# Kernel tuning notes

Hardware: AMD Instinct MI355X
Metric: run time of the kernel (lower is better)

Reference implementation:

```python
import jax, jax.numpy as jnp
import numpy as np

B, N, C, C_OUT, E = 8, 1024, 256, 256, 16384


def setup_inputs() -> dict:
    key = jax.random.key(0)
    k1, k2, k3 = jax.random.split(key, 3)
    x = jax.random.normal(k1, (B, N, C), dtype=jnp.float32)
    edge_index = jax.random.randint(k2, (2, E, B), 0, N)  # [2, E, B], values in [0, N)
    W = jax.random.normal(k3, (C_OUT, C), dtype=jnp.float32) * 0.02  # torch Linear weight [out, in]
    b = jnp.zeros((C_OUT,), dtype=jnp.float32)
    return {"x": x, "edge_index": edge_index, "W": W, "b": b}


def reference(x, edge_index, W, b):
    Bs, Nn, Cc = x.shape
    BN = Bs * Nn
    # Vectorized version of the per-batch python loop: offset each graph's
    # node indices into the big block-diagonal adjacency.
    offs = jnp.arange(Bs, dtype=edge_index.dtype) * Nn          # [B]
    src = (edge_index[0] + offs[None, :]).reshape(-1)           # [E*B]
    dst = (edge_index[1] + offs[None, :]).reshape(-1)           # [E*B]
    adj = jnp.zeros((BN, BN), dtype=x.dtype).at[src, dst].set(1.0)
    adj = adj + jnp.eye(BN, dtype=x.dtype)                      # self loops (adds on top, as in torch code)
    D = adj.sum(axis=1)                                         # [BN]
    d_inv_sqrt = jnp.where(D > 0, jax.lax.rsqrt(D), 0.0)        # pow(-0.5) with inf -> 0
    adj_n = d_inv_sqrt[:, None] * adj * d_inv_sqrt[None, :]     # D^-1/2 A D^-1/2
    h = adj_n @ x.reshape(BN, Cc)                               # [BN, C]
    out = h @ W.T + b                                           # Linear
    return out.reshape(Bs, Nn, -1)
```

## Files before the change

### kernel.cpp

```cpp
#include <hip/hip_runtime.h>
#include <stdint.h>

#define B_   8
#define N_   1024
#define C_   256
#define E_   16384
#define BN_  (B_ * N_)
#define NW_  (N_ / 32)
#define LIST_CAP 96

typedef __attribute__((ext_vector_type(8))) short bf16x8;
typedef __attribute__((ext_vector_type(4))) float f32x4;

static __device__ __forceinline__ short f32_to_bf16(float f) {
  uint32_t u = __float_as_uint(f);
  uint32_t r = (u + 0x7fffu + ((u >> 16) & 1u)) >> 16;
  return (short)r;
}
static __device__ __forceinline__ float bf16_to_f32(short s) {
  return __uint_as_float(((uint32_t)(uint16_t)s) << 16);
}

__global__ __launch_bounds__(256) void gemm_scatter(
    const float* __restrict__ X, const float* __restrict__ W,
    const int* __restrict__ ei, uint32_t* __restrict__ mask,
    float* __restrict__ Y) {
  __shared__ __attribute__((aligned(16))) short Ah[64][40];
  __shared__ __attribute__((aligned(16))) short Al[64][40];
  __shared__ __attribute__((aligned(16))) short Bh[64][40];
  __shared__ __attribute__((aligned(16))) short Bl[64][40];

  int t  = threadIdx.x;
  int m0 = blockIdx.x * 64;
  int n0 = blockIdx.y * 64;

  {
    int e   = (blockIdx.y * gridDim.x + blockIdx.x) * 256 + t;
    int b   = e & (B_ - 1);
    int src = ei[e];
    int dst = ei[E_ * B_ + e];
    atomicOr(&mask[(size_t)(b * N_ + src) * NW_ + (dst >> 5)],
             1u << (dst & 31));
  }

  int lr = t >> 2;
  int lc = (t & 3) * 8;
  int wv = t >> 6;
  int ln = t & 63;
  int lm = ln & 15;
  int qd = ln >> 4;

  f32x4 acc[4];
#pragma unroll
  for (int i = 0; i < 4; i++) acc[i] = (f32x4){0.f, 0.f, 0.f, 0.f};

  for (int k0 = 0; k0 < C_; k0 += 32) {
    const float* xr = &X[(size_t)(m0 + lr) * C_ + k0 + lc];
    const float* wr = &W[(size_t)(n0 + lr) * C_ + k0 + lc];
    float xv[8], wv8[8];
    *(float4*)&xv[0] = *(const float4*)&xr[0];
    *(float4*)&xv[4] = *(const float4*)&xr[4];
    *(float4*)&wv8[0] = *(const float4*)&wr[0];
    *(float4*)&wv8[4] = *(const float4*)&wr[4];
    bf16x8 xh, xl, wh, wl;
#pragma unroll
    for (int j = 0; j < 8; j++) {
      short h = f32_to_bf16(xv[j]);
      xh[j] = h;
      xl[j] = f32_to_bf16(xv[j] - bf16_to_f32(h));
      short g = f32_to_bf16(wv8[j]);
      wh[j] = g;
      wl[j] = f32_to_bf16(wv8[j] - bf16_to_f32(g));
    }
    __syncthreads();
    *(bf16x8*)&Ah[lr][lc] = xh;
    *(bf16x8*)&Al[lr][lc] = xl;
    *(bf16x8*)&Bh[lr][lc] = wh;
    *(bf16x8*)&Bl[lr][lc] = wl;
    __syncthreads();

    bf16x8 ah = *(const bf16x8*)&Ah[16 * wv + lm][qd * 8];
    bf16x8 al = *(const bf16x8*)&Al[16 * wv + lm][qd * 8];
#pragma unroll
    for (int nt = 0; nt < 4; nt++) {
      bf16x8 bh = *(const bf16x8*)&Bh[nt * 16 + lm][qd * 8];
      bf16x8 bl = *(const bf16x8*)&Bl[nt * 16 + lm][qd * 8];
      acc[nt] = __builtin_amdgcn_mfma_f32_16x16x32_bf16(ah, bh, acc[nt], 0, 0, 0);
      acc[nt] = __builtin_amdgcn_mfma_f32_16x16x32_bf16(ah, bl, acc[nt], 0, 0, 0);
      acc[nt] = __builtin_amdgcn_mfma_f32_16x16x32_bf16(al, bh, acc[nt], 0, 0, 0);
    }
  }

#pragma unroll
  for (int nt = 0; nt < 4; nt++) {
#pragma unroll
    for (int r = 0; r < 4; r++) {
      int m = m0 + 16 * wv + qd * 4 + r;
      int n = n0 + nt * 16 + lm;
      Y[(size_t)m * C_ + n] = acc[nt][r];
    }
  }
}

__global__ __launch_bounds__(256) void aggregate(
    const uint32_t* __restrict__ mask, const float* __restrict__ Y,
    const float* __restrict__ bias, float* __restrict__ out) {
  __shared__ uint16_t lists[4][LIST_CAP];
  __shared__ float    wgts[4][LIST_CAP];

  int blk   = blockIdx.x;
  int batch = blk & 7;
  int group = blk >> 3;
  int wv    = threadIdx.x >> 6;
  int ln    = threadIdx.x & 63;
  int loc   = group * 4 + wv;
  int node  = batch * N_ + loc;
  int c4    = ln * 4;

  const uint32_t* mb = mask + (size_t)batch * N_ * NW_;

  uint32_t bits = (ln < NW_) ? mb[(size_t)loc * NW_ + ln] : 0u;
  int cnt = __popc(bits);
  int pfx = cnt;
#pragma unroll
  for (int off = 1; off < 64; off <<= 1) {
    int v = __shfl_up(pfx, off);
    if (ln >= off) pfx += v;
  }
  int total = __shfl(pfx, 63);
  pfx -= cnt;
  uint16_t* lst = lists[wv];
  float*    wgt = wgts[wv];
  int o = pfx, jb = ln * 32;
  while (bits) {
    int j = __ffs(bits) - 1;
    bits &= bits - 1;
    lst[o++] = (uint16_t)(jb + j);
  }
  if (ln == 0) {
    int dd = total;
    while (dd & 3) { lst[dd] = 0; wgt[dd] = 0.f; dd++; }
  }

  int half = ln >> 5;
  int wl   = ln & 31;
  for (int k = 0; k < total; k += 2) {
    int kk = k + half;
    int nj = (kk < total) ? lst[kk] : 0;
    int p  = __popc(mb[(size_t)nj * NW_ + wl]);
    p += __shfl_xor(p, 1);  p += __shfl_xor(p, 2);  p += __shfl_xor(p, 4);
    p += __shfl_xor(p, 8);  p += __shfl_xor(p, 16);
    if (wl == 0 && kk < total) wgt[kk] = rsqrtf((float)(p + 1));
  }

  const float* yb = Y + (size_t)batch * N_ * C_;
  float di = rsqrtf((float)(total + 1));
  float4 s = *(const float4*)&yb[(size_t)loc * C_ + c4];
  float4 acc;
  acc.x = di * s.x; acc.y = di * s.y; acc.z = di * s.z; acc.w = di * s.w;

  for (int k = 0; k < total; k += 4) {
    ushort4 n4 = *(const ushort4*)&lst[k];
    float4  w4 = *(const float4*)&wgt[k];
    float4 z0 = *(const float4*)&yb[(size_t)n4.x * C_ + c4];
    float4 z1 = *(const float4*)&yb[(size_t)n4.y * C_ + c4];
    float4 z2 = *(const float4*)&yb[(size_t)n4.z * C_ + c4];
    float4 z3 = *(const float4*)&yb[(size_t)n4.w * C_ + c4];
    acc.x += w4.x * z0.x; acc.y += w4.x * z0.y; acc.z += w4.x * z0.z; acc.w += w4.x * z0.w;
    acc.x += w4.y * z1.x; acc.y += w4.y * z1.y; acc.z += w4.y * z1.z; acc.w += w4.y * z1.w;
    acc.x += w4.z * z2.x; acc.y += w4.z * z2.y; acc.z += w4.z * z2.z; acc.w += w4.z * z2.w;
    acc.x += w4.w * z3.x; acc.y += w4.w * z3.y; acc.z += w4.w * z3.z; acc.w += w4.w * z3.w;
  }

  float4 bb = *(const float4*)&bias[c4];
  float4 o4;
  o4.x = di * acc.x + bb.x;
  o4.y = di * acc.y + bb.y;
  o4.z = di * acc.z + bb.z;
  o4.w = di * acc.w + bb.w;
  *(float4*)&out[(size_t)node * C_ + c4] = o4;
}

extern "C" void kernel_launch(void* const* d_in, const int* in_sizes, int n_in,
                              void* d_out, int out_size, void* d_ws,
                              size_t ws_size, hipStream_t stream) {
  const float* x    = (const float*)d_in[0];
  const int*   ei   = (const int*)d_in[1];
  const float* W    = (const float*)d_in[2];
  const float* bias = (const float*)d_in[3];
  float*       out  = (float*)d_out;

  char* ws = (char*)d_ws;
  uint32_t* mask = (uint32_t*)(ws + 0x000000);
  float*    Y    = (float*)   (ws + 0x100000);

  hipMemsetAsync(mask, 0, (size_t)BN_ * NW_ * 4, stream);

  gemm_scatter<<<dim3(BN_ / 64, C_ / 64), 256, 0, stream>>>(x, W, ei, mask, Y);
  aggregate<<<BN_ / 4, 256, 0, stream>>>(mask, Y, bias, out);
}
```

Measured before the change: 97.29 us.

## Fuse memset, GEMM/scatter and aggregation into one cooperative kernel with grid syncs

Replaces the memset plus two kernel launches with a single cooperative kernel of 512 blocks. Each block first zeroes part of the adjacency bitmask, then does the edge scatter and a GEMM tile, and after a grid sync loops over four virtual aggregation blocks. This removes launch and inter-kernel gaps. In exchange it adds grid-wide barrier costs and cuts the aggregation phase to a fixed 512-block grid with serialized iterations.

```diff
diff --git a/kernel.cpp b/kernel.cpp
--- a/kernel.cpp
+++ b/kernel.cpp
@@ -1,5 +1,8 @@
 #include <hip/hip_runtime.h>
+#include <hip/hip_cooperative_groups.h>
 #include <stdint.h>
+
+namespace cg = cooperative_groups;
 
 #define B_   8
 #define N_   1024
@@ -8,6 +11,7 @@
 #define BN_  (B_ * N_)
 #define NW_  (N_ / 32)
 #define LIST_CAP 96
+#define GRID_ 512
 
 typedef __attribute__((ext_vector_type(8))) short bf16x8;
 typedef __attribute__((ext_vector_type(4))) float f32x4;
@@ -21,28 +25,36 @@
   return __uint_as_float(((uint32_t)(uint16_t)s) << 16);
 }
 
-__global__ __launch_bounds__(256) void gemm_scatter(
+__global__ __launch_bounds__(256, 2) void gcn_fused(
     const float* __restrict__ X, const float* __restrict__ W,
-    const int* __restrict__ ei, uint32_t* __restrict__ mask,
-    float* __restrict__ Y) {
+    const int* __restrict__ ei, const float* __restrict__ bias,
+    uint32_t* __restrict__ mask, float* __restrict__ Y,
+    float* __restrict__ out) {
   __shared__ __attribute__((aligned(16))) short Ah[64][40];
   __shared__ __attribute__((aligned(16))) short Al[64][40];
   __shared__ __attribute__((aligned(16))) short Bh[64][40];
   __shared__ __attribute__((aligned(16))) short Bl[64][40];
-
-  int t  = threadIdx.x;
-  int m0 = blockIdx.x * 64;
-  int n0 = blockIdx.y * 64;
+  __shared__ uint16_t lists[4][LIST_CAP];
+  __shared__ float    wgts[4][LIST_CAP];
+
+  cg::grid_group grid = cg::this_grid();
+  int t   = threadIdx.x;
+  int tid = blockIdx.x * 256 + t;
+
+  ((uint2*)mask)[tid] = make_uint2(0u, 0u);
+  __threadfence();
+  grid.sync();
 
   {
-    int e   = (blockIdx.y * gridDim.x + blockIdx.x) * 256 + t;
-    int b   = e & (B_ - 1);
-    int src = ei[e];
-    int dst = ei[E_ * B_ + e];
+    int b   = tid & (B_ - 1);
+    int src = ei[tid];
+    int dst = ei[E_ * B_ + tid];
     atomicOr(&mask[(size_t)(b * N_ + src) * NW_ + (dst >> 5)],
              1u << (dst & 31));
   }
 
+  int m0 = (blockIdx.x >> 2) * 64;
+  int n0 = (blockIdx.x & 3) * 64;
   int lr = t >> 2;
   int lc = (t & 3) * 8;
   int wv = t >> 6;
@@ -100,85 +112,82 @@
       Y[(size_t)m * C_ + n] = acc[nt][r];
     }
   }
-}
-
-__global__ __launch_bounds__(256) void aggregate(
-    const uint32_t* __restrict__ mask, const float* __restrict__ Y,
-    const float* __restrict__ bias, float* __restrict__ out) {
-  __shared__ uint16_t lists[4][LIST_CAP];
-  __shared__ float    wgts[4][LIST_CAP];
-
-  int blk   = blockIdx.x;
-  int batch = blk & 7;
-  int group = blk >> 3;
-  int wv    = threadIdx.x >> 6;
-  int ln    = threadIdx.x & 63;
-  int loc   = group * 4 + wv;
-  int node  = batch * N_ + loc;
-  int c4    = ln * 4;
-
-  const uint32_t* mb = mask + (size_t)batch * N_ * NW_;
-
-  uint32_t bits = (ln < NW_) ? mb[(size_t)loc * NW_ + ln] : 0u;
-  int cnt = __popc(bits);
-  int pfx = cnt;
-#pragma unroll
-  for (int off = 1; off < 64; off <<= 1) {
-    int v = __shfl_up(pfx, off);
-    if (ln >= off) pfx += v;
-  }
-  int total = __shfl(pfx, 63);
-  pfx -= cnt;
-  uint16_t* lst = lists[wv];
-  float*    wgt = wgts[wv];
-  int o = pfx, jb = ln * 32;
-  while (bits) {
-    int j = __ffs(bits) - 1;
-    bits &= bits - 1;
-    lst[o++] = (uint16_t)(jb + j);
-  }
-  if (ln == 0) {
-    int dd = total;
-    while (dd & 3) { lst[dd] = 0; wgt[dd] = 0.f; dd++; }
-  }
-
-  int half = ln >> 5;
-  int wl   = ln & 31;
-  for (int k = 0; k < total; k += 2) {
-    int kk = k + half;
-    int nj = (kk < total) ? lst[kk] : 0;
-    int p  = __popc(mb[(size_t)nj * NW_ + wl]);
-    p += __shfl_xor(p, 1);  p += __shfl_xor(p, 2);  p += __shfl_xor(p, 4);
-    p += __shfl_xor(p, 8);  p += __shfl_xor(p, 16);
-    if (wl == 0 && kk < total) wgt[kk] = rsqrtf((float)(p + 1));
-  }
-
-  const float* yb = Y + (size_t)batch * N_ * C_;
-  float di = rsqrtf((float)(total + 1));
-  float4 s = *(const float4*)&yb[(size_t)loc * C_ + c4];
-  float4 acc;
-  acc.x = di * s.x; acc.y = di * s.y; acc.z = di * s.z; acc.w = di * s.w;
-
-  for (int k = 0; k < total; k += 4) {
-    ushort4 n4 = *(const ushort4*)&lst[k];
-    float4  w4 = *(const float4*)&wgt[k];
-    float4 z0 = *(const float4*)&yb[(size_t)n4.x * C_ + c4];
-    float4 z1 = *(const float4*)&yb[(size_t)n4.y * C_ + c4];
-    float4 z2 = *(const float4*)&yb[(size_t)n4.z * C_ + c4];
-    float4 z3 = *(const float4*)&yb[(size_t)n4.w * C_ + c4];
-    acc.x += w4.x * z0.x; acc.y += w4.x * z0.y; acc.z += w4.x * z0.z; acc.w += w4.x * z0.w;
-    acc.x += w4.y * z1.x; acc.y += w4.y * z1.y; acc.z += w4.y * z1.z; acc.w += w4.y * z1.w;
-    acc.x += w4.z * z2.x; acc.y += w4.z * z2.y; acc.z += w4.z * z2.z; acc.w += w4.z * z2.w;
-    acc.x += w4.w * z3.x; acc.y += w4.w * z3.y; acc.z += w4.w * z3.z; acc.w += w4.w * z3.w;
-  }
-
-  float4 bb = *(const float4*)&bias[c4];
-  float4 o4;
-  o4.x = di * acc.x + bb.x;
-  o4.y = di * acc.y + bb.y;
-  o4.z = di * acc.z + bb.z;
-  o4.w = di * acc.w + bb.w;
-  *(float4*)&out[(size_t)node * C_ + c4] = o4;
+
+  __threadfence();
+  grid.sync();
+  __threadfence();
+
+  for (int it = 0; it < 4; it++) {
+    int vblk  = it * GRID_ + blockIdx.x;
+    int batch = vblk & 7;
+    int group = vblk >> 3;
+    int loc   = group * 4 + wv;
+    int node  = batch * N_ + loc;
+    int c4    = ln * 4;
+
+    const uint32_t* mb = mask + (size_t)batch * N_ * NW_;
+
+    uint32_t bits = (ln < NW_) ? mb[(size_t)loc * NW_ + ln] : 0u;
+    int cnt = __popc(bits);
+    int pfx = cnt;
+#pragma unroll
+    for (int off = 1; off < 64; off <<= 1) {
+      int v = __shfl_up(pfx, off);
+      if (ln >= off) pfx += v;
+    }
+    int total = __shfl(pfx, 63);
+    pfx -= cnt;
+    uint16_t* lst = lists[wv];
+    float*    wgt = wgts[wv];
+    int o = pfx, jb = ln * 32;
+    while (bits) {
+      int j = __ffs(bits) - 1;
+      bits &= bits - 1;
+      lst[o++] = (uint16_t)(jb + j);
+    }
+    if (ln == 0) {
+      int dd = total;
+      while (dd & 3) { lst[dd] = 0; wgt[dd] = 0.f; dd++; }
+    }
+
+    int half = ln >> 5;
+    int wl   = ln & 31;
+    for (int k = 0; k < total; k += 2) {
+      int kk = k + half;
+      int nj = (kk < total) ? lst[kk] : 0;
+      int p  = __popc(mb[(size_t)nj * NW_ + wl]);
+      p += __shfl_xor(p, 1);  p += __shfl_xor(p, 2);  p += __shfl_xor(p, 4);
+      p += __shfl_xor(p, 8);  p += __shfl_xor(p, 16);
+      if (wl == 0 && kk < total) wgt[kk] = rsqrtf((float)(p + 1));
+    }
+
+    const float* yb = Y + (size_t)batch * N_ * C_;
+    float di = rsqrtf((float)(total + 1));
+    float4 s = *(const float4*)&yb[(size_t)loc * C_ + c4];
+    float4 a4;
+    a4.x = di * s.x; a4.y = di * s.y; a4.z = di * s.z; a4.w = di * s.w;
+
+    for (int k = 0; k < total; k += 4) {
+      ushort4 n4 = *(const ushort4*)&lst[k];
+      float4  w4 = *(const float4*)&wgt[k];
+      float4 z0 = *(const float4*)&yb[(size_t)n4.x * C_ + c4];
+      float4 z1 = *(const float4*)&yb[(size_t)n4.y * C_ + c4];
+      float4 z2 = *(const float4*)&yb[(size_t)n4.z * C_ + c4];
+      float4 z3 = *(const float4*)&yb[(size_t)n4.w * C_ + c4];
+      a4.x += w4.x * z0.x; a4.y += w4.x * z0.y; a4.z += w4.x * z0.z; a4.w += w4.x * z0.w;
+      a4.x += w4.y * z1.x; a4.y += w4.y * z1.y; a4.z += w4.y * z1.z; a4.w += w4.y * z1.w;
+      a4.x += w4.z * z2.x; a4.y += w4.z * z2.y; a4.z += w4.z * z2.z; a4.w += w4.z * z2.w;
+      a4.x += w4.w * z3.x; a4.y += w4.w * z3.y; a4.z += w4.w * z3.z; a4.w += w4.w * z3.w;
+    }
+
+    float4 bb = *(const float4*)&bias[c4];
+    float4 o4;
+    o4.x = di * a4.x + bb.x;
+    o4.y = di * a4.y + bb.y;
+    o4.z = di * a4.z + bb.z;
+    o4.w = di * a4.w + bb.w;
+    *(float4*)&out[(size_t)node * C_ + c4] = o4;
+  }
 }
 
 extern "C" void kernel_launch(void* const* d_in, const int* in_sizes, int n_in,
@@ -194,8 +203,8 @@
   uint32_t* mask = (uint32_t*)(ws + 0x000000);
   float*    Y    = (float*)   (ws + 0x100000);
 
-  hipMemsetAsync(mask, 0, (size_t)BN_ * NW_ * 4, stream);
-
-  gemm_scatter<<<dim3(BN_ / 64, C_ / 64), 256, 0, stream>>>(x, W, ei, mask, Y);
-  aggregate<<<BN_ / 4, 256, 0, stream>>>(mask, Y, bias, out);
-}
+  void* args[] = {(void*)&x, (void*)&W, (void*)&ei, (void*)&bias,
+                  (void*)&mask, (void*)&Y, (void*)&out};
+  hipLaunchCooperativeKernel((void*)gcn_fused, dim3(GRID_), dim3(256),
+                             args, 0, stream);
+}
```

After: 318.8 us. 3.28x slower.
